# Kernel optimization log

Measured on AMD Instinct MI355X. Metric: run time of the kernel, lower is better.

The kernel has to match this reference:

```python
import jax, jax.numpy as jnp
import numpy as np

B, N, C, O = 1, 8192, 256, 64


def setup_inputs() -> dict:
    key = jax.random.key(0)
    ks = jax.random.split(key, 7)
    return {
        "x": jax.random.normal(ks[0], (B, N, C), dtype=jnp.float32),
        "W1": jax.random.normal(ks[1], (O, C), dtype=jnp.float32) * 0.05,
        "b1": jax.random.normal(ks[2], (O,), dtype=jnp.float32) * 0.05,
        "a1": jax.random.normal(ks[3], (O,), dtype=jnp.float32) * 0.05,
        "ba1": jax.random.normal(ks[4], (1,), dtype=jnp.float32) * 0.05,
        "a2": jax.random.normal(ks[5], (O,), dtype=jnp.float32) * 0.05,
        "ba2": jax.random.normal(ks[6], (1,), dtype=jnp.float32) * 0.05,
    }


def reference(x, W1, b1, a1, ba1, a2, ba2):
    # conv1 (1x1 Conv1d) == per-node linear: seq_fts [B, O, N]
    seq_fts = jnp.einsum('bnc,oc->bon', x, W1) + b1[None, :, None]
    # conv2_1 / conv2_2 (O -> 1, 1x1): f1, f2 [B, N]
    f1 = jnp.einsum('bon,o->bn', seq_fts, a1) + ba1
    f2 = jnp.einsum('bon,o->bn', seq_fts, a2) + ba2
    # logits[b,i,j] = f1[b,i] + f2[b,j]  -> [B, N, N]
    logits = jax.nn.leaky_relu(f1[:, :, None] + f2[:, None, :], negative_slope=0.01)
    # NOTE: original uses nn.Softmax(dim=1) on [B, N, N] -> normalize over axis 1
    coefs = jax.nn.softmax(logits, axis=1)
    # ret[b,i,o] = sum_j coefs[b,i,j] * seq_fts[b,o,j]  -> [B, N, O]
    ret = jnp.einsum('bij,boj->bio', coefs, seq_fts)
    return jax.nn.elu(ret)
```

## Files before the change

### kernel.cpp

```cpp
#include <hip/hip_runtime.h>
#include <math.h>

#define NN 8192
#define CC 256
#define OO 64
#define JW 8

__global__ __launch_bounds__(256) void k_gemm(
    const float* __restrict__ x, const float* __restrict__ W1,
    const float* __restrict__ b1, const float* __restrict__ a1,
    const float* __restrict__ ba1, const float* __restrict__ a2,
    const float* __restrict__ ba2,
    float* __restrict__ seq,
    float* __restrict__ f1, float* __restrict__ f2,
    float* __restrict__ E1, float* __restrict__ E1s,
    float* __restrict__ eF2, float* __restrict__ eF2s,
    unsigned long long* __restrict__ keys )
{
  __shared__ float w_lds[64][66];
  __shared__ float x_lds[16][256];
  const int t = threadIdx.x;
  const int p = t & 31;
  const int g = t >> 5;
  const int r0 = blockIdx.x*16 + g*2;
  const int r1 = r0 + 1;
  {
    const float4* xg = (const float4*)(x + (size_t)blockIdx.x*16*CC);
#pragma unroll
    for (int q = t; q < 1024; q += 256)
      ((float4*)x_lds)[q] = xg[q];
  }
  float c00 = 0.f, c01 = 0.f, c10 = 0.f, c11 = 0.f;
  for (int ct = 0; ct < 4; ++ct) {
    __syncthreads();
    for (int idx = t; idx < 4096; idx += 256) {
      const int o = idx >> 6, cc = idx & 63;
      w_lds[cc][o] = W1[o*CC + ct*64 + cc];
    }
    __syncthreads();
    const float* xr0 = &x_lds[g*2][ct*64];
    const float* xr1 = &x_lds[g*2+1][ct*64];
#pragma unroll 4
    for (int c = 0; c < 64; c += 4) {
      const float4 xa = *(const float4*)(xr0 + c);
      const float4 xb = *(const float4*)(xr1 + c);
      const float2 w0 = *(const float2*)&w_lds[c+0][2*p];
      const float2 w1 = *(const float2*)&w_lds[c+1][2*p];
      const float2 w2 = *(const float2*)&w_lds[c+2][2*p];
      const float2 w3 = *(const float2*)&w_lds[c+3][2*p];
      c00 = fmaf(xa.x, w0.x, c00); c00 = fmaf(xa.y, w1.x, c00);
      c00 = fmaf(xa.z, w2.x, c00); c00 = fmaf(xa.w, w3.x, c00);
      c01 = fmaf(xa.x, w0.y, c01); c01 = fmaf(xa.y, w1.y, c01);
      c01 = fmaf(xa.z, w2.y, c01); c01 = fmaf(xa.w, w3.y, c01);
      c10 = fmaf(xb.x, w0.x, c10); c10 = fmaf(xb.y, w1.x, c10);
      c10 = fmaf(xb.z, w2.x, c10); c10 = fmaf(xb.w, w3.x, c10);
      c11 = fmaf(xb.x, w0.y, c11); c11 = fmaf(xb.y, w1.y, c11);
      c11 = fmaf(xb.z, w2.y, c11); c11 = fmaf(xb.w, w3.y, c11);
    }
  }
  const float2 B2 = *(const float2*)&b1[2*p];
  const float v00 = c00 + B2.x, v01 = c01 + B2.y;
  const float v10 = c10 + B2.x, v11 = c11 + B2.y;
  *(float2*)&seq[(size_t)r0*OO + 2*p] = make_float2(v00, v01);
  *(float2*)&seq[(size_t)r1*OO + 2*p] = make_float2(v10, v11);
  const float2 A1 = *(const float2*)&a1[2*p];
  const float2 A2 = *(const float2*)&a2[2*p];
  float p1_0 = v00*A1.x + v01*A1.y;
  float p2_0 = v00*A2.x + v01*A2.y;
  float p1_1 = v10*A1.x + v11*A1.y;
  float p2_1 = v10*A2.x + v11*A2.y;
#pragma unroll
  for (int d = 1; d < 32; d <<= 1) {
    p1_0 += __shfl_xor(p1_0, d, 64);
    p2_0 += __shfl_xor(p2_0, d, 64);
    p1_1 += __shfl_xor(p1_1, d, 64);
    p2_1 += __shfl_xor(p2_1, d, 64);
  }
  if (p == 0) {
    const float bba1 = ba1[0], bba2 = ba2[0];
    const float t1a = p1_0 + bba1, t2a = p2_0 + bba2;
    const float t1b = p1_1 + bba1, t2b = p2_1 + bba2;
    f1[r0] = t1a; E1[r0] = expf(t1a); E1s[r0] = expf(0.01f*t1a);
    f2[r0] = t2a; eF2[r0] = expf(t2a); eF2s[r0] = expf(0.01f*t2a);
    f1[r1] = t1b; E1[r1] = expf(t1b); E1s[r1] = expf(0.01f*t1b);
    f2[r1] = t2b; eF2[r1] = expf(t2b); eF2s[r1] = expf(0.01f*t2b);
    unsigned u;
    u = __float_as_uint(t1a); u = (u & 0x80000000u) ? ~u : (u | 0x80000000u);
    keys[r0] = ((unsigned long long)u << 32) | (unsigned)r0;
    u = __float_as_uint(t1b); u = (u & 0x80000000u) ? ~u : (u | 0x80000000u);
    keys[r1] = ((unsigned long long)u << 32) | (unsigned)r1;
    u = __float_as_uint(t2a); u = (u & 0x80000000u) ? ~u : (u | 0x80000000u);
    keys[NN + r0] = ((unsigned long long)u << 32) | (unsigned)r0;
    u = __float_as_uint(t2b); u = (u & 0x80000000u) ? ~u : (u | 0x80000000u);
    keys[NN + r1] = ((unsigned long long)u << 32) | (unsigned)r1;
  }
}

__global__ __launch_bounds__(512) void k_rank(
    const unsigned long long* __restrict__ keys,
    const float* __restrict__ f1, const float* __restrict__ E1,
    const float* __restrict__ E1s, const float* __restrict__ f2,
    const float* __restrict__ eF2, const float* __restrict__ eF2s,
    float* __restrict__ s1, float* __restrict__ se1, float* __restrict__ se1s,
    int* __restrict__ inv1,
    float* __restrict__ f2s, float* __restrict__ eF2srt,
    float* __restrict__ eF2ssrt, int* __restrict__ inv)
{
  __shared__ unsigned long long skl[NN];
  const int t = threadIdx.x;
  const int lane = t & 63, wv = t >> 6;
  const int gw = blockIdx.x*8 + wv;
  const int bj = gw*JW;
  const int arr = bj >> 13;
  const int jb = bj & (NN-1);
  const unsigned long long* kb = keys + ((size_t)arr << 13);
  for (int q = t; q < NN/2; q += 512)
    ((ulonglong2*)skl)[q] = ((const ulonglong2*)kb)[q];
  __syncthreads();
  unsigned long long K[JW];
#pragma unroll
  for (int q = 0; q < JW; ++q) {
    const unsigned long long kk = skl[jb + q];
    const unsigned lo = __builtin_amdgcn_readfirstlane((unsigned)kk);
    const unsigned hi = __builtin_amdgcn_readfirstlane((unsigned)(kk >> 32));
    K[q] = ((unsigned long long)hi << 32) | lo;
  }
  int cnt[JW];
#pragma unroll
  for (int q = 0; q < JW; ++q) cnt[q] = 0;
#pragma unroll 4
  for (int c = 0; c < NN/64; ++c) {
    const unsigned long long sk = skl[c*64 + lane];
#pragma unroll
    for (int q = 0; q < JW; ++q)
      cnt[q] += (sk < K[q]) ? 1 : 0;
  }
#pragma unroll
  for (int q = 0; q < JW; ++q) {
    int r = cnt[q];
#pragma unroll
    for (int d = 1; d < 64; d <<= 1) r += __shfl_xor(r, d, 64);
    if (lane == 0) {
      const int i = jb + q;
      if (arr == 0) {
        s1[r] = f1[i]; se1[r] = E1[i]; se1s[r] = E1s[i]; inv1[r] = i;
      } else {
        inv[r] = i; f2s[r] = f2[i]; eF2srt[r] = eF2[i]; eF2ssrt[r] = eF2s[i];
      }
    }
  }
}

__global__ __launch_bounds__(1024) void k_DT(
    const float* __restrict__ se1, const float* __restrict__ se1s,
    const float* __restrict__ s1g,
    const float* __restrict__ f2s, const float* __restrict__ eF2srt,
    const float* __restrict__ eF2ssrt, const int* __restrict__ inv,
    const float* __restrict__ seq,
    float* __restrict__ Bs, float* __restrict__ Es,
    int* __restrict__ kpos, float* __restrict__ TU, float* __restrict__ TV)
{
  __shared__ float s1l[NN];
  __shared__ float f2sl[NN];
  __shared__ float csA[256], csB[256];
  __shared__ float csEA[257], csEB[257];
  __shared__ float wsA[4], wsB[4];
  __shared__ float bsl[32], esl[32];
  __shared__ float redU[16][64], redV[16][64];
  const int t = threadIdx.x;
  const int b = blockIdx.x;
  const int wv = t >> 6, lane = t & 63;
  const float4 a0 = ((const float4*)se1 )[t*2];
  const float4 a1v = ((const float4*)se1 )[t*2+1];
  const float4 b0 = ((const float4*)se1s)[t*2];
  const float4 b1v = ((const float4*)se1s)[t*2+1];
  ((float4*)s1l)[t*2]   = ((const float4*)s1g)[t*2];
  ((float4*)s1l)[t*2+1] = ((const float4*)s1g)[t*2+1];
  ((float4*)f2sl)[t*2]   = ((const float4*)f2s)[t*2];
  ((float4*)f2sl)[t*2+1] = ((const float4*)f2s)[t*2+1];
  float sa = ((a0.x+a0.y)+(a0.z+a0.w)) + ((a1v.x+a1v.y)+(a1v.z+a1v.w));
  float sb = ((b0.x+b0.y)+(b0.z+b0.w)) + ((b1v.x+b1v.y)+(b1v.z+b1v.w));
  sa += __shfl_xor(sa, 1, 64); sb += __shfl_xor(sb, 1, 64);
  sa += __shfl_xor(sa, 2, 64); sb += __shfl_xor(sb, 2, 64);
  if ((t & 3) == 0) { csA[t>>2] = sa; csB[t>>2] = sb; }
  __syncthreads();
  if (t < 256) {
    float a = csA[t], bv = csB[t];
#pragma unroll
    for (int d = 1; d < 64; d <<= 1) {
      const float ua = __shfl_up(a, d, 64);
      const float ub = __shfl_up(bv, d, 64);
      if (lane >= d) { a += ua; bv += ub; }
    }
    csA[t] = a; csB[t] = bv;
    if (lane == 63) { wsA[wv] = a; wsB[wv] = bv; }
  }
  __syncthreads();
  if (t < 256) {
    float baseA = 0.f, baseB = 0.f;
    for (int q = 0; q < wv; ++q) { baseA += wsA[q]; baseB += wsB[q]; }
    csEA[t+1] = csA[t] + baseA;
    csEB[t+1] = csB[t] + baseB;
    if (t == 0) { csEA[0] = 0.f; csEB[0] = 0.f; }
  }
  __syncthreads();
  const int half = lane >> 5, m = lane & 31;
  {
    const int kk = b*32 + 2*wv + half;
    const float tgt = -f2sl[kk];
    int pos = 0;
#pragma unroll
    for (int s = NN; s; s >>= 1) {
      const int c = pos + s;
      if (c <= NN && s1l[c-1] < tgt) pos = c;
    }
    const int base = pos & ~31, cn = pos & 31;
    float ta = 0.f, tb = 0.f;
    if (m < cn) { ta = se1[base+m]; tb = se1s[base+m]; }
#pragma unroll
    for (int d = 1; d < 32; d <<= 1) {
      ta += __shfl_xor(ta, d, 64);
      tb += __shfl_xor(tb, d, 64);
    }
    if (m == 0) {
      const float PreA = csEA[pos>>5] + ta;
      const float PreB = csEB[pos>>5] + tb;
      const float T1 = csEA[256];
      const float e2 = eF2srt[kk], e2s = eF2ssrt[kk];
      const float D = fmaf(T1 - PreA, e2, PreB * e2s);
      const float bsv = e2 / D, esv = e2s / D;
      Bs[kk] = bsv; Es[kk] = esv;
      bsl[2*wv + half] = bsv; esl[2*wv + half] = esv;
    }
  }
  if (t < 32) {
    const int r = b*32 + t;
    const float tgt = -s1l[r];
    int pos = 0;
#pragma unroll
    for (int s = NN; s; s >>= 1) {
      const int c = pos + s;
      if (c <= NN && f2sl[c-1] < tgt) pos = c;
    }
    kpos[r] = pos;
  }
  __syncthreads();
  {
    const int kk0 = b*32 + 2*wv, kk1 = kk0 + 1;
    const float s0v = seq[(size_t)inv[kk0]*OO + lane];
    const float s1v = seq[(size_t)inv[kk1]*OO + lane];
    redU[wv][lane] = bsl[2*wv]*s0v + bsl[2*wv+1]*s1v;
    redV[wv][lane] = esl[2*wv]*s0v + esl[2*wv+1]*s1v;
  }
  __syncthreads();
  if (wv == 0) {
    float r = 0.f;
#pragma unroll
    for (int q = 0; q < 16; ++q) r += redU[q][lane];
    TU[b*64 + lane] = r;
  } else if (wv == 1) {
    float r = 0.f;
#pragma unroll
    for (int q = 0; q < 16; ++q) r += redV[q][lane];
    TV[b*64 + lane] = r;
  }
}

__global__ __launch_bounds__(1024) void k_merge(
    const int* __restrict__ kpos, const int* __restrict__ inv,
    const int* __restrict__ inv1,
    const float* __restrict__ se1, const float* __restrict__ se1s,
    const float* __restrict__ Bs, const float* __restrict__ Es,
    const float* __restrict__ seq,
    const float* __restrict__ TU, const float* __restrict__ TV,
    float* __restrict__ out)
{
  __shared__ int kposl[NN];
  __shared__ float pu[33][64], pv[33][64];
  __shared__ float rA[16][64], rB[16][64], rC[16][64];
  __shared__ int bnd[2];
  const int t = threadIdx.x, lane = t & 63, wv = t >> 6, b = blockIdx.x;
  for (int q = t; q < NN/4; q += 1024)
    ((int4*)kposl)[q] = ((const int4*)kpos)[q];
  float pbu = 0.f, pbv = 0.f, ptu = 0.f;
  for (int c = wv; c < 256; c += 16) {
    const float tu = TU[c*64 + lane], tv = TV[c*64 + lane];
    ptu += tu;
    if (c < b) { pbu += tu; pbv += tv; }
  }
  rA[wv][lane] = pbu; rB[wv][lane] = pbv; rC[wv][lane] = ptu;
  {
    const int kk0 = b*32 + 2*wv, kk1 = kk0 + 1;
    const float sv0 = seq[(size_t)inv[kk0]*OO + lane];
    const float sv1 = seq[(size_t)inv[kk1]*OO + lane];
    pu[2*wv+1][lane] = Bs[kk0]*sv0; pv[2*wv+1][lane] = Es[kk0]*sv0;
    pu[2*wv+2][lane] = Bs[kk1]*sv1; pv[2*wv+2][lane] = Es[kk1]*sv1;
  }
  if (wv == 0) { pu[0][lane] = 0.f; pv[0][lane] = 0.f; }
  __syncthreads();
  if (t == 0) {
    const int hi = 32*b + 32 + (b == 255 ? 1 : 0);
    int pos = 0;
    for (int s = NN; s; s >>= 1) { const int c = pos+s; if (c <= NN && kposl[c-1] >= hi) pos = c; }
    bnd[0] = pos;
    pos = 0;
    const int lo = 32*b;
    for (int s = NN; s; s >>= 1) { const int c = pos+s; if (c <= NN && kposl[c-1] >= lo) pos = c; }
    bnd[1] = pos;
  }
  float base_u = 0.f, base_v = 0.f, utot = 0.f;
#pragma unroll
  for (int q = 0; q < 16; ++q) {
    base_u += rA[q][lane]; base_v += rB[q][lane]; utot += rC[q][lane];
  }
  for (int d = 1; d < 32; d <<= 1) {
    const int rowA = wv + 1;
    const int rowB = wv + 17;
    const int srcA = rowA - d, srcB = rowB - d;
    const float aA = (srcA >= 0) ? pu[srcA][lane] : 0.f;
    const float vA = (srcA >= 0) ? pv[srcA][lane] : 0.f;
    const float aB = (srcB >= 0) ? pu[srcB][lane] : 0.f;
    const float vB = (srcB >= 0) ? pv[srcB][lane] : 0.f;
    __syncthreads();
    pu[rowA][lane] += aA; pv[rowA][lane] += vA;
    pu[rowB][lane] += aB; pv[rowB][lane] += vB;
    __syncthreads();
  }
  const int r0 = bnd[0], r1 = bnd[1];
  for (int r = r0 + wv; r < r1; r += 16) {
    const int kl = kposl[r] - 32*b;
    const float ret = se1[r]*(utot - (base_u + pu[kl][lane]))
                    + se1s[r]*(base_v + pv[kl][lane]);
    out[(size_t)inv1[r]*OO + lane] = (ret > 0.f) ? ret : expm1f(ret);
  }
}

extern "C" void kernel_launch(void* const* d_in, const int* in_sizes, int n_in,
                              void* d_out, int out_size, void* d_ws, size_t ws_size,
                              hipStream_t stream)
{
  (void)in_sizes; (void)n_in; (void)out_size; (void)ws_size;
  const float* x   = (const float*)d_in[0];
  const float* W1  = (const float*)d_in[1];
  const float* b1  = (const float*)d_in[2];
  const float* a1  = (const float*)d_in[3];
  const float* ba1 = (const float*)d_in[4];
  const float* a2  = (const float*)d_in[5];
  const float* ba2 = (const float*)d_in[6];
  float* out = (float*)d_out;

  float* w = (float*)d_ws;
  size_t off = 0;
  auto alloc = [&](size_t n) { float* p = w + off; off += (n + 63) & ~(size_t)63; return p; };
  float* seq  = alloc((size_t)NN*OO);
  float* f1   = alloc(NN);
  float* f2   = alloc(NN);
  float* E1   = alloc(NN);
  float* E1s  = alloc(NN);
  float* eF2  = alloc(NN);
  float* eF2s = alloc(NN);
  unsigned long long* keys = (unsigned long long*)alloc((size_t)4*NN);
  int*   inv1 = (int*)alloc(NN);
  int*   inv  = (int*)alloc(NN);
  float* s1   = alloc(NN);
  float* se1  = alloc(NN);
  float* se1s = alloc(NN);
  float* f2s  = alloc(NN);
  float* eF2srt  = alloc(NN);
  float* eF2ssrt = alloc(NN);
  float* Bs   = alloc(NN);
  float* Es   = alloc(NN);
  int*   kpos = (int*)alloc(NN);
  float* TU   = alloc(256*64);
  float* TV   = alloc(256*64);

  k_gemm<<<512, 256, 0, stream>>>(x, W1, b1, a1, ba1, a2, ba2,
                                  seq, f1, f2, E1, E1s, eF2, eF2s, keys);
  k_rank<<<256, 512, 0, stream>>>(keys, f1, E1, E1s, f2, eF2, eF2s,
                                  s1, se1, se1s, inv1, f2s, eF2srt, eF2ssrt, inv);
  k_DT<<<256, 1024, 0, stream>>>(se1, se1s, s1, f2s, eF2srt, eF2ssrt,
                                 inv, seq, Bs, Es, kpos, TU, TV);
  k_merge<<<256, 1024, 0, stream>>>(kpos, inv, inv1, se1, se1s, Bs, Es,
                                    seq, TU, TV, out);
}
```

Before: 53.83 us.

## Split GEMM over K and rank counting over key halves for more parallelism

The projection GEMM is split along the channel dimension into two halves on a 2-D grid, writing partial results that a new k_fsum kernel adds together. k_fsum also applies the bias, computes f1/f2, their exponentials and the sort keys. The rank kernel is likewise split so each block counts against only half of the keys, holding half as much shared memory. A new k_scat kernel sums the two partial counts and scatters the sorted arrays. This doubles the block count for the GEMM and rank stages to fill more compute units, at the cost of two extra launches and extra global traffic for the partial results.

```diff
diff --git a/kernel.cpp b/kernel.cpp
--- a/kernel.cpp
+++ b/kernel.cpp
@@ -8,34 +8,27 @@
 
 __global__ __launch_bounds__(256) void k_gemm(
     const float* __restrict__ x, const float* __restrict__ W1,
-    const float* __restrict__ b1, const float* __restrict__ a1,
-    const float* __restrict__ ba1, const float* __restrict__ a2,
-    const float* __restrict__ ba2,
-    float* __restrict__ seq,
-    float* __restrict__ f1, float* __restrict__ f2,
-    float* __restrict__ E1, float* __restrict__ E1s,
-    float* __restrict__ eF2, float* __restrict__ eF2s,
-    unsigned long long* __restrict__ keys )
+    float* __restrict__ seqp )
 {
   __shared__ float w_lds[64][66];
-  __shared__ float x_lds[16][256];
+  __shared__ float x_lds[16][128];
   const int t = threadIdx.x;
   const int p = t & 31;
   const int g = t >> 5;
-  const int r0 = blockIdx.x*16 + g*2;
+  const int bx = blockIdx.x, h = blockIdx.y;
+  const int r0 = bx*16 + g*2;
   const int r1 = r0 + 1;
-  {
-    const float4* xg = (const float4*)(x + (size_t)blockIdx.x*16*CC);
-#pragma unroll
-    for (int q = t; q < 1024; q += 256)
-      ((float4*)x_lds)[q] = xg[q];
+  for (int q = t; q < 512; q += 256) {
+    const int row = q >> 5, c4 = q & 31;
+    ((float4*)x_lds[row])[c4] =
+        ((const float4*)(x + (size_t)(bx*16 + row)*CC + h*128))[c4];
   }
   float c00 = 0.f, c01 = 0.f, c10 = 0.f, c11 = 0.f;
-  for (int ct = 0; ct < 4; ++ct) {
+  for (int ct = 0; ct < 2; ++ct) {
     __syncthreads();
     for (int idx = t; idx < 4096; idx += 256) {
       const int o = idx >> 6, cc = idx & 63;
-      w_lds[cc][o] = W1[o*CC + ct*64 + cc];
+      w_lds[cc][o] = W1[o*CC + h*128 + ct*64 + cc];
     }
     __syncthreads();
     const float* xr0 = &x_lds[g*2][ct*64];
@@ -58,46 +51,88 @@
       c11 = fmaf(xb.z, w2.y, c11); c11 = fmaf(xb.w, w3.y, c11);
     }
   }
-  const float2 B2 = *(const float2*)&b1[2*p];
-  const float v00 = c00 + B2.x, v01 = c01 + B2.y;
-  const float v10 = c10 + B2.x, v11 = c11 + B2.y;
-  *(float2*)&seq[(size_t)r0*OO + 2*p] = make_float2(v00, v01);
-  *(float2*)&seq[(size_t)r1*OO + 2*p] = make_float2(v10, v11);
-  const float2 A1 = *(const float2*)&a1[2*p];
-  const float2 A2 = *(const float2*)&a2[2*p];
-  float p1_0 = v00*A1.x + v01*A1.y;
-  float p2_0 = v00*A2.x + v01*A2.y;
-  float p1_1 = v10*A1.x + v11*A1.y;
-  float p2_1 = v10*A2.x + v11*A2.y;
-#pragma unroll
-  for (int d = 1; d < 32; d <<= 1) {
-    p1_0 += __shfl_xor(p1_0, d, 64);
-    p2_0 += __shfl_xor(p2_0, d, 64);
-    p1_1 += __shfl_xor(p1_1, d, 64);
-    p2_1 += __shfl_xor(p2_1, d, 64);
-  }
-  if (p == 0) {
-    const float bba1 = ba1[0], bba2 = ba2[0];
-    const float t1a = p1_0 + bba1, t2a = p2_0 + bba2;
-    const float t1b = p1_1 + bba1, t2b = p2_1 + bba2;
-    f1[r0] = t1a; E1[r0] = expf(t1a); E1s[r0] = expf(0.01f*t1a);
-    f2[r0] = t2a; eF2[r0] = expf(t2a); eF2s[r0] = expf(0.01f*t2a);
-    f1[r1] = t1b; E1[r1] = expf(t1b); E1s[r1] = expf(0.01f*t1b);
-    f2[r1] = t2b; eF2[r1] = expf(t2b); eF2s[r1] = expf(0.01f*t2b);
+  float* dst = seqp + (size_t)h*NN*OO;
+  *(float2*)&dst[(size_t)r0*OO + 2*p] = make_float2(c00, c01);
+  *(float2*)&dst[(size_t)r1*OO + 2*p] = make_float2(c10, c11);
+}
+
+__global__ __launch_bounds__(256) void k_fsum(
+    const float* __restrict__ seqp, const float* __restrict__ b1,
+    const float* __restrict__ a1, const float* __restrict__ ba1,
+    const float* __restrict__ a2, const float* __restrict__ ba2,
+    float* __restrict__ seq,
+    float* __restrict__ f1, float* __restrict__ f2,
+    float* __restrict__ E1, float* __restrict__ E1s,
+    float* __restrict__ eF2, float* __restrict__ eF2s,
+    unsigned long long* __restrict__ keys)
+{
+  const int lane = threadIdx.x & 63;
+  const int i = blockIdx.x*4 + (threadIdx.x >> 6);
+  const float s = seqp[(size_t)i*OO + lane]
+                + seqp[(size_t)(NN + i)*OO + lane] + b1[lane];
+  seq[(size_t)i*OO + lane] = s;
+  float p1 = s * a1[lane];
+  float p2 = s * a2[lane];
+#pragma unroll
+  for (int d = 1; d < 64; d <<= 1) {
+    p1 += __shfl_xor(p1, d, 64);
+    p2 += __shfl_xor(p2, d, 64);
+  }
+  if (lane == 0) {
+    const float t1 = p1 + ba1[0], t2 = p2 + ba2[0];
+    f1[i] = t1; E1[i] = expf(t1); E1s[i] = expf(0.01f*t1);
+    f2[i] = t2; eF2[i] = expf(t2); eF2s[i] = expf(0.01f*t2);
     unsigned u;
-    u = __float_as_uint(t1a); u = (u & 0x80000000u) ? ~u : (u | 0x80000000u);
-    keys[r0] = ((unsigned long long)u << 32) | (unsigned)r0;
-    u = __float_as_uint(t1b); u = (u & 0x80000000u) ? ~u : (u | 0x80000000u);
-    keys[r1] = ((unsigned long long)u << 32) | (unsigned)r1;
-    u = __float_as_uint(t2a); u = (u & 0x80000000u) ? ~u : (u | 0x80000000u);
-    keys[NN + r0] = ((unsigned long long)u << 32) | (unsigned)r0;
-    u = __float_as_uint(t2b); u = (u & 0x80000000u) ? ~u : (u | 0x80000000u);
-    keys[NN + r1] = ((unsigned long long)u << 32) | (unsigned)r1;
+    u = __float_as_uint(t1); u = (u & 0x80000000u) ? ~u : (u | 0x80000000u);
+    keys[i] = ((unsigned long long)u << 32) | (unsigned)i;
+    u = __float_as_uint(t2); u = (u & 0x80000000u) ? ~u : (u | 0x80000000u);
+    keys[NN + i] = ((unsigned long long)u << 32) | (unsigned)i;
   }
 }
 
 __global__ __launch_bounds__(512) void k_rank(
-    const unsigned long long* __restrict__ keys,
+    const unsigned long long* __restrict__ keys, int* __restrict__ pCnt)
+{
+  __shared__ unsigned long long skl[NN/2];
+  const int t = threadIdx.x;
+  const int lane = t & 63, wv = t >> 6;
+  const int bx = blockIdx.x, kh = blockIdx.y;
+  const int arr = bx >> 7;
+  const int jbw = (bx & 127)*64 + wv*JW;
+  const unsigned long long* kb = keys + ((size_t)arr << 13);
+  for (int q = t; q < NN/4; q += 512)
+    ((ulonglong2*)skl)[q] = ((const ulonglong2*)(kb + kh*(NN/2)))[q];
+  __syncthreads();
+  unsigned long long K[JW];
+#pragma unroll
+  for (int q = 0; q < JW; ++q) {
+    const unsigned long long kk = kb[jbw + q];
+    const unsigned lo = __builtin_amdgcn_readfirstlane((unsigned)kk);
+    const unsigned hi = __builtin_amdgcn_readfirstlane((unsigned)(kk >> 32));
+    K[q] = ((unsigned long long)hi << 32) | lo;
+  }
+  int cnt[JW];
+#pragma unroll
+  for (int q = 0; q < JW; ++q) cnt[q] = 0;
+#pragma unroll 4
+  for (int c = 0; c < NN/128; ++c) {
+    const unsigned long long sk = skl[c*64 + lane];
+#pragma unroll
+    for (int q = 0; q < JW; ++q)
+      cnt[q] += (sk < K[q]) ? 1 : 0;
+  }
+#pragma unroll
+  for (int q = 0; q < JW; ++q) {
+    int r = cnt[q];
+#pragma unroll
+    for (int d = 1; d < 64; d <<= 1) r += __shfl_xor(r, d, 64);
+    if (lane == 0)
+      pCnt[(size_t)(arr*2 + kh)*NN + jbw + q] = r;
+  }
+}
+
+__global__ __launch_bounds__(512) void k_scat(
+    const int* __restrict__ pCnt,
     const float* __restrict__ f1, const float* __restrict__ E1,
     const float* __restrict__ E1s, const float* __restrict__ f2,
     const float* __restrict__ eF2, const float* __restrict__ eF2s,
@@ -106,48 +141,13 @@
     float* __restrict__ f2s, float* __restrict__ eF2srt,
     float* __restrict__ eF2ssrt, int* __restrict__ inv)
 {
-  __shared__ unsigned long long skl[NN];
-  const int t = threadIdx.x;
-  const int lane = t & 63, wv = t >> 6;
-  const int gw = blockIdx.x*8 + wv;
-  const int bj = gw*JW;
-  const int arr = bj >> 13;
-  const int jb = bj & (NN-1);
-  const unsigned long long* kb = keys + ((size_t)arr << 13);
-  for (int q = t; q < NN/2; q += 512)
-    ((ulonglong2*)skl)[q] = ((const ulonglong2*)kb)[q];
-  __syncthreads();
-  unsigned long long K[JW];
-#pragma unroll
-  for (int q = 0; q < JW; ++q) {
-    const unsigned long long kk = skl[jb + q];
-    const unsigned lo = __builtin_amdgcn_readfirstlane((unsigned)kk);
-    const unsigned hi = __builtin_amdgcn_readfirstlane((unsigned)(kk >> 32));
-    K[q] = ((unsigned long long)hi << 32) | lo;
-  }
-  int cnt[JW];
-#pragma unroll
-  for (int q = 0; q < JW; ++q) cnt[q] = 0;
-#pragma unroll 4
-  for (int c = 0; c < NN/64; ++c) {
-    const unsigned long long sk = skl[c*64 + lane];
-#pragma unroll
-    for (int q = 0; q < JW; ++q)
-      cnt[q] += (sk < K[q]) ? 1 : 0;
-  }
-#pragma unroll
-  for (int q = 0; q < JW; ++q) {
-    int r = cnt[q];
-#pragma unroll
-    for (int d = 1; d < 64; d <<= 1) r += __shfl_xor(r, d, 64);
-    if (lane == 0) {
-      const int i = jb + q;
-      if (arr == 0) {
-        s1[r] = f1[i]; se1[r] = E1[i]; se1s[r] = E1s[i]; inv1[r] = i;
-      } else {
-        inv[r] = i; f2s[r] = f2[i]; eF2srt[r] = eF2[i]; eF2ssrt[r] = eF2s[i];
-      }
-    }
+  const int u = blockIdx.x*512 + threadIdx.x;
+  const int arr = u >> 13, j = u & (NN-1);
+  const int r = pCnt[(size_t)(arr*2)*NN + j] + pCnt[(size_t)(arr*2+1)*NN + j];
+  if (arr == 0) {
+    s1[r] = f1[j]; se1[r] = E1[j]; se1s[r] = E1s[j]; inv1[r] = j;
+  } else {
+    inv[r] = j; f2s[r] = f2[j]; eF2srt[r] = eF2[j]; eF2ssrt[r] = eF2s[j];
   }
 }
 
@@ -352,6 +352,7 @@
   float* w = (float*)d_ws;
   size_t off = 0;
   auto alloc = [&](size_t n) { float* p = w + off; off += (n + 63) & ~(size_t)63; return p; };
+  float* seqp = alloc((size_t)2*NN*OO);
   float* seq  = alloc((size_t)NN*OO);
   float* f1   = alloc(NN);
   float* f2   = alloc(NN);
@@ -360,6 +361,7 @@
   float* eF2  = alloc(NN);
   float* eF2s = alloc(NN);
   unsigned long long* keys = (unsigned long long*)alloc((size_t)4*NN);
+  int*   pCnt = (int*)alloc((size_t)4*NN);
   int*   inv1 = (int*)alloc(NN);
   int*   inv  = (int*)alloc(NN);
   float* s1   = alloc(NN);
@@ -374,10 +376,12 @@
   float* TU   = alloc(256*64);
   float* TV   = alloc(256*64);
 
-  k_gemm<<<512, 256, 0, stream>>>(x, W1, b1, a1, ba1, a2, ba2,
-                                  seq, f1, f2, E1, E1s, eF2, eF2s, keys);
-  k_rank<<<256, 512, 0, stream>>>(keys, f1, E1, E1s, f2, eF2, eF2s,
-                                  s1, se1, se1s, inv1, f2s, eF2srt, eF2ssrt, inv);
+  k_gemm<<<dim3(512, 2), 256, 0, stream>>>(x, W1, seqp);
+  k_fsum<<<2048, 256, 0, stream>>>(seqp, b1, a1, ba1, a2, ba2,
+                                   seq, f1, f2, E1, E1s, eF2, eF2s, keys);
+  k_rank<<<dim3(256, 2), 512, 0, stream>>>(keys, pCnt);
+  k_scat<<<32, 512, 0, stream>>>(pCnt, f1, E1, E1s, f2, eF2, eF2s,
+                                 s1, se1, se1s, inv1, f2s, eF2srt, eF2ssrt, inv);
   k_DT<<<256, 1024, 0, stream>>>(se1, se1s, s1, f2s, eF2srt, eF2ssrt,
                                  inv, seq, Bs, Es, kpos, TU, TV);
   k_merge<<<256, 1024, 0, stream>>>(kpos, inv, inv1, se1, se1s, Bs, Es,
```

Measured after the change: 55.30 us. 1.03x slower.
